# Kernel optimization log

Measured on AMD Instinct MI355X. Metric: run time of the kernel, lower is better.

## Reference

```python
import jax, jax.numpy as jnp
import numpy as np

N = 2_000_000
N_IN = 128
N_HID = 32
CT_SIZE = 16384  # n_bags(1024) * n_ct(16)
N_CT = 16


def setup_inputs() -> dict:
    key = jax.random.key(0)
    ks = jax.random.split(key, 10)
    X = jax.random.normal(ks[0], (N, N_IN), dtype=jnp.float32)
    batch = jax.random.randint(ks[1], (N,), 0, CT_SIZE, dtype=jnp.int32)
    s = 1.0 / np.sqrt(N_IN)
    W1 = jax.random.uniform(ks[2], (N_IN, N_HID), jnp.float32, -s, s)
    b1 = jax.random.uniform(ks[3], (N_HID,), jnp.float32, -s, s)
    s2 = 1.0 / np.sqrt(N_HID)
    wc = jax.random.uniform(ks[4], (N_HID, 1), jnp.float32, -s2, s2)
    bc = jax.random.uniform(ks[5], (1,), jnp.float32, -s2, s2)
    wct = jax.random.uniform(ks[6], (N_HID, 1), jnp.float32, -s2, s2)
    bct = jax.random.uniform(ks[7], (1,), jnp.float32, -s2, s2)
    Wout = jax.random.uniform(ks[8], (N_HID, 1), jnp.float32, -s2, s2)
    bout = jax.random.uniform(ks[9], (1,), jnp.float32, -s2, s2)
    return {"X": X, "W1": W1, "b1": b1, "wc": wc, "bc": bc,
            "wct": wct, "bct": bct, "Wout": Wout, "bout": bout,
            "batch": batch, "ct_size": CT_SIZE, "n_ct": N_CT}


def _segment_softmax(s, batch, num_segments):
    # numerically stable softmax within each segment
    m = jax.ops.segment_max(s, batch, num_segments=num_segments)
    e = jnp.exp(s - m[batch])
    denom = jax.ops.segment_sum(e, batch, num_segments=num_segments)
    return e / denom[batch]


def reference(X, W1, b1, wc, bc, wct, bct, Wout, bout, batch, ct_size, n_ct):
    # lin: Linear(n_in, n_hid) + ReLU (dropout=0 in eval)
    H = jax.nn.relu(X @ W1 + b1)                          # [N, n_hid]
    # attn1 with use_softmax: segment softmax over cells within each (bag, celltype) segment
    s = (H @ wc + bc)[:, 0]                               # [N]
    w_c = _segment_softmax(s, batch, ct_size)             # [N]
    # global_add_pool of attention-weighted features, reshape to [n_bags, n_ct, n_hid]
    P = jax.ops.segment_sum(H * w_c[:, None], batch, num_segments=ct_size)
    P = P.reshape(-1, n_ct, N_HID)                        # [B, n_ct, n_hid]
    # lin2 is empty (n_layers_lin2=0)
    # attn2: softmax over cell-type axis
    w_ct = jax.nn.softmax(P @ wct + bct, axis=1)          # [B, n_ct, 1]
    Xb = jnp.sum(P * w_ct, axis=1)                        # [B, n_hid]
    return Xb @ Wout + bout                               # [B, 1]
```

## Files before the change

### kernel.cpp

```cpp
#include <hip/hip_runtime.h>
#include <hip/hip_bf16.h>
#include <cmath>

#define NIN   128
#define NHID  32
#define CTS   16384
#define NCT   16
#define NBAGS (CTS / NCT)
#define CAP   256
#define NBLK  256
#define SEG_STRIDE 33

typedef __attribute__((ext_vector_type(8))) short bf16x8;
typedef __attribute__((ext_vector_type(4))) float f32x4;

__device__ inline ushort f2bf(float f) {
    uint x = __float_as_uint(f);
    uint r = (x + 0x7fffu + ((x >> 16) & 1u)) >> 16;
    return (ushort)r;
}
__device__ inline float bf2f(ushort b) { return __uint_as_float(((uint)b) << 16); }


__global__ __launch_bounds__(1024) void hist_kernel(
    const int* __restrict__ batch, uint* __restrict__ hist, int n, int chunk)
{
    __shared__ uint h[CTS];
    const int b = blockIdx.x;
    for (int i = threadIdx.x; i < CTS; i += 1024) h[i] = 0;
    __syncthreads();
    const int lo = b * chunk, hi = min(n, lo + chunk);
    for (int i = lo + threadIdx.x; i < hi; i += 1024)
        atomicAdd(&h[batch[i]], 1u);
    __syncthreads();
    uint* __restrict__ hb = hist + (size_t)b * CTS;
    for (int i = threadIdx.x; i < CTS; i += 1024) hb[i] = h[i];
}

__global__ __launch_bounds__(256) void prefix_kernel(
    uint* __restrict__ hist, int* __restrict__ cnt)
{
    const int s = blockIdx.x * 256 + threadIdx.x;
    if (s >= CTS) return;
    uint run = 0;
#pragma unroll 4
    for (int b = 0; b < NBLK; ++b) {
        const uint t = hist[(size_t)b * CTS + s];
        hist[(size_t)b * CTS + s] = run;
        run += t;
    }
    cnt[s * 16] = (int)run;
}

__global__ __launch_bounds__(1024) void place_kernel(
    const int* __restrict__ batch, const uint* __restrict__ hist,
    int* __restrict__ slots, int n, int chunk)
{
    __shared__ uint h[CTS];
    const int b = blockIdx.x;
    const uint* __restrict__ hb = hist + (size_t)b * CTS;
    for (int i = threadIdx.x; i < CTS; i += 1024) h[i] = hb[i];
    __syncthreads();
    const int lo = b * chunk, hi = min(n, lo + chunk);
    for (int i = lo + threadIdx.x; i < hi; i += 1024) {
        const int s = batch[i];
        const uint pos = atomicAdd(&h[s], 1u);
        if (pos < CAP) slots[(size_t)s * CAP + pos] = i;
    }
}

__global__ __launch_bounds__(256) void seg_kernel(
    const float* __restrict__ X,
    const float* __restrict__ W1,
    const float* __restrict__ b1,
    const float* __restrict__ wc,
    const float* __restrict__ bc,
    const int*   __restrict__ cnt,
    const int*   __restrict__ slots,
    float* __restrict__ P)
{
    __shared__ __align__(16) float w1s[NIN * NHID];

    const int tid = threadIdx.x;
    for (int i = tid; i < NIN * NHID / 4; i += 256)
        ((float4*)w1s)[i] = ((const float4*)W1)[i];
    __syncthreads();

    const int w    = tid >> 6;
    const int lane = tid & 63;
    const int g    = lane >> 4;
    const int c    = lane & 15;
    const int s    = blockIdx.x * 4 + w;
    const int m    = min(cnt[s * 16], CAP);

    bf16x8 Bf[4][2];
#pragma unroll
    for (int kc = 0; kc < 4; ++kc) {
#pragma unroll
        for (int nh = 0; nh < 2; ++nh) {
            union { bf16x8 v; ushort u[8]; } bh;
#pragma unroll
            for (int e = 0; e < 8; ++e)
                bh.u[e] = f2bf(w1s[(kc * 32 + g * 8 + e) * NHID + nh * 16 + c]);
            Bf[kc][nh] = bh.v;
        }
    }

    const float b1c0 = b1[c], b1c1 = b1[c + 16];
    const float wc0  = wc[c], wc1  = wc[c + 16];
    const float bc0  = bc[0];

    float pacc0 = 0.f, pacc1 = 0.f, esum = 0.f;
    const int ntiles = (m + 15) >> 4;
    const size_t sbase = (size_t)s * CAP;

    auto slot_of = [&](int t) -> int {
        const int ti = t * 16 + c;
        return slots[sbase + min(ti, m - 1)];
    };

    auto compute_tile = [&](const float4* x, int t) {
        f32x4 acc0 = {0.f, 0.f, 0.f, 0.f};
        f32x4 acc1 = {0.f, 0.f, 0.f, 0.f};
#pragma unroll
        for (int kc = 0; kc < 4; ++kc) {
            const float xs[8] = {x[2*kc].x, x[2*kc].y, x[2*kc].z, x[2*kc].w,
                                 x[2*kc+1].x, x[2*kc+1].y, x[2*kc+1].z, x[2*kc+1].w};
            union { bf16x8 v; __hip_bfloat162 h2[4]; } ah, al;
            float lo[8];
#pragma unroll
            for (int e = 0; e < 4; ++e) {
                const __hip_bfloat162 hb =
                    __float22bfloat162_rn(make_float2(xs[2*e], xs[2*e+1]));
                ah.h2[e] = hb;
                lo[2*e]   = xs[2*e]   - __bfloat162float(hb.x);
                lo[2*e+1] = xs[2*e+1] - __bfloat162float(hb.y);
            }
#pragma unroll
            for (int e = 0; e < 4; ++e)
                al.h2[e] = __float22bfloat162_rn(make_float2(lo[2*e], lo[2*e+1]));

            acc0 = __builtin_amdgcn_mfma_f32_16x16x32_bf16(ah.v, Bf[kc][0], acc0, 0, 0, 0);
            acc0 = __builtin_amdgcn_mfma_f32_16x16x32_bf16(al.v, Bf[kc][0], acc0, 0, 0, 0);
            acc1 = __builtin_amdgcn_mfma_f32_16x16x32_bf16(ah.v, Bf[kc][1], acc1, 0, 0, 0);
            acc1 = __builtin_amdgcn_mfma_f32_16x16x32_bf16(al.v, Bf[kc][1], acc1, 0, 0, 0);
        }
#pragma unroll
        for (int i = 0; i < 4; ++i) {
            const float h0 = fmaxf(acc0[i] + b1c0, 0.f);
            const float h1 = fmaxf(acc1[i] + b1c1, 0.f);
            float sp = h0 * wc0 + h1 * wc1;
            sp += __shfl_xor(sp, 1);
            sp += __shfl_xor(sp, 2);
            sp += __shfl_xor(sp, 4);
            sp += __shfl_xor(sp, 8);
            const int row = t * 16 + g * 4 + i;
            const float e = (row < m) ? expf(sp + bc0) : 0.f;
            pacc0 = fmaf(e, h0, pacc0);
            pacc1 = fmaf(e, h1, pacc1);
            esum += e;
        }
    };

    auto load_tile = [&](float4* x, int r) {
        const float4* __restrict__ xr = (const float4*)(X + (size_t)r * NIN);
#pragma unroll
        for (int kc = 0; kc < 4; ++kc) {
            x[2*kc]   = xr[kc * 8 + g * 2];
            x[2*kc+1] = xr[kc * 8 + g * 2 + 1];
        }
    };

    if (ntiles > 0) {
        float4 xa[8];
        load_tile(xa, slot_of(0));
        int rnext = (ntiles > 1) ? slot_of(1) : 0;

        for (int t = 0; t < ntiles; ++t) {
            float4 xb[8];
            const bool more = (t + 1) < ntiles;
            if (more) load_tile(xb, rnext);
            const int rnn = (t + 2 < ntiles) ? slot_of(t + 2) : 0;
            compute_tile(xa, t);
#pragma unroll
            for (int q = 0; q < 8; ++q) xa[q] = xb[q];
            rnext = rnn;
        }
    }

    pacc0 += __shfl_xor(pacc0, 16); pacc0 += __shfl_xor(pacc0, 32);
    pacc1 += __shfl_xor(pacc1, 16); pacc1 += __shfl_xor(pacc1, 32);
    esum  += __shfl_xor(esum, 16);  esum  += __shfl_xor(esum, 32);

    if (lane < 16) {
        const float inv = esum > 0.f ? 1.f / esum : 0.f;
        P[(size_t)s * NHID + c]      = pacc0 * inv;
        P[(size_t)s * NHID + 16 + c] = pacc1 * inv;
    }
}

__global__ __launch_bounds__(256) void bags_kernel(
    const float* __restrict__ P,
    const float* __restrict__ wct,
    const float* __restrict__ bct,
    const float* __restrict__ Wout,
    const float* __restrict__ bout,
    float* __restrict__ out)
{
    const int b = blockIdx.x * blockDim.x + threadIdx.x;
    if (b >= NBAGS) return;

    float logit[NCT], dout[NCT];
#pragma unroll
    for (int ct = 0; ct < NCT; ++ct) {
        const float* p = P + (size_t)(b * NCT + ct) * NHID;
        float t = 0.f, d = 0.f;
#pragma unroll
        for (int j = 0; j < NHID; ++j) {
            const float pj = p[j];
            t += pj * wct[j];
            d += pj * Wout[j];
        }
        logit[ct] = t + bct[0];
        dout[ct]  = d;
    }

    float mx = logit[0];
#pragma unroll
    for (int ct = 1; ct < NCT; ++ct) mx = fmaxf(mx, logit[ct]);
    float den = 0.f, accv = 0.f;
#pragma unroll
    for (int ct = 0; ct < NCT; ++ct) {
        const float e = expf(logit[ct] - mx);
        den += e;
        accv += e * dout[ct];
    }
    out[b] = accv / den + bout[0];
}


__global__ __launch_bounds__(256) void rows_kernel_atomic(
    const float* __restrict__ X, const float* __restrict__ W1,
    const float* __restrict__ b1, const float* __restrict__ wc,
    const float* __restrict__ bc, const int* __restrict__ batch,
    float* __restrict__ segacc, int n)
{
    const long long r0 = (long long)blockIdx.x * 256 + threadIdx.x;
    if (r0 >= n) return;
    const float4* xp = (const float4*)(X + (size_t)r0 * NIN);
    float acc[NHID];
#pragma unroll
    for (int j = 0; j < NHID; ++j) acc[j] = 0.f;
#pragma unroll 4
    for (int kc = 0; kc < NIN / 4; ++kc) {
        const float4 xv = xp[kc];
        const float xa[4] = {xv.x, xv.y, xv.z, xv.w};
#pragma unroll
        for (int kk = 0; kk < 4; ++kk) {
            const float* wrow = W1 + (kc * 4 + kk) * NHID;
            const float u = xa[kk];
#pragma unroll
            for (int j = 0; j < NHID; ++j) acc[j] = fmaf(u, wrow[j], acc[j]);
        }
    }
    float sc = bc[0];
#pragma unroll
    for (int j = 0; j < NHID; ++j) {
        const float h = fmaxf(acc[j] + b1[j], 0.f); acc[j] = h; sc += h * wc[j];
    }
    const float e = expf(sc);
    float* p = segacc + (size_t)batch[r0] * SEG_STRIDE;
#pragma unroll
    for (int j = 0; j < NHID; ++j) atomicAdd(p + j, e * acc[j]);
    atomicAdd(p + NHID, e);
}

__global__ __launch_bounds__(256) void bags_kernel_fb(
    const float* __restrict__ segacc, const float* __restrict__ wct,
    const float* __restrict__ bct, const float* __restrict__ Wout,
    const float* __restrict__ bout, float* __restrict__ out)
{
    const int b = blockIdx.x * blockDim.x + threadIdx.x;
    if (b >= NBAGS) return;
    float logit[NCT], dout[NCT];
#pragma unroll
    for (int ct = 0; ct < NCT; ++ct) {
        const float* p = segacc + (size_t)(b * NCT + ct) * SEG_STRIDE;
        const float den = p[NHID];
        const float inv = den > 0.f ? 1.f / den : 0.f;
        float t = 0.f, d = 0.f;
#pragma unroll
        for (int j = 0; j < NHID; ++j) { const float pj = p[j]*inv; t += pj*wct[j]; d += pj*Wout[j]; }
        logit[ct] = t + bct[0];
        dout[ct]  = d;
    }
    float mx = logit[0];
#pragma unroll
    for (int ct = 1; ct < NCT; ++ct) mx = fmaxf(mx, logit[ct]);
    float den = 0.f, accv = 0.f;
#pragma unroll
    for (int ct = 0; ct < NCT; ++ct) {
        const float e = expf(logit[ct] - mx);
        den += e; accv += e * dout[ct];
    }
    out[b] = accv / den + bout[0];
}


extern "C" void kernel_launch(void* const* d_in, const int* in_sizes, int n_in,
                              void* d_out, int out_size, void* d_ws, size_t ws_size,
                              hipStream_t stream)
{
    const float* X    = (const float*)d_in[0];
    const float* W1   = (const float*)d_in[1];
    const float* b1   = (const float*)d_in[2];
    const float* wc   = (const float*)d_in[3];
    const float* bc   = (const float*)d_in[4];
    const float* wct  = (const float*)d_in[5];
    const float* bct  = (const float*)d_in[6];
    const float* Wout = (const float*)d_in[7];
    const float* bout = (const float*)d_in[8];
    const int*   batch= (const int*)d_in[9];
    const int n = in_sizes[9];

    const size_t cnt_bytes  = (size_t)CTS * 16 * sizeof(int);
    const size_t slot_bytes = (size_t)CTS * CAP * sizeof(int);
    const size_t p_bytes    = (size_t)CTS * NHID * sizeof(float);
    const size_t hist_bytes = (size_t)NBLK * CTS * sizeof(uint);
    const size_t need = cnt_bytes + slot_bytes + p_bytes + hist_bytes;

    if (ws_size >= need) {
        int*   cnt   = (int*)d_ws;
        int*   slots = cnt + (size_t)CTS * 16;
        float* P     = (float*)(slots + (size_t)CTS * CAP);
        uint*  hist  = (uint*)(P + (size_t)CTS * NHID);

        const int chunk = (n + NBLK - 1) / NBLK;
        hist_kernel<<<NBLK, 1024, 0, stream>>>(batch, hist, n, chunk);
        prefix_kernel<<<CTS / 256, 256, 0, stream>>>(hist, cnt);
        place_kernel<<<NBLK, 1024, 0, stream>>>(batch, hist, slots, n, chunk);
        seg_kernel<<<CTS / 4, 256, 0, stream>>>(X, W1, b1, wc, bc, cnt, slots, P);
        bags_kernel<<<(NBAGS + 255) / 256, 256, 0, stream>>>(
            P, wct, bct, Wout, bout, (float*)d_out);
    } else {
        float* segacc = (float*)d_ws;
        hipMemsetAsync(segacc, 0, (size_t)CTS * SEG_STRIDE * sizeof(float), stream);
        rows_kernel_atomic<<<(n + 255) / 256, 256, 0, stream>>>(
            X, W1, b1, wc, bc, batch, segacc, n);
        bags_kernel_fb<<<(NBAGS + 255) / 256, 256, 0, stream>>>(
            segacc, wct, bct, Wout, bout, (float*)d_out);
    }
}
```

Baseline: 298.8 us.

## Stream X coalesced, scatter bf16 hidden rows by segment, reduce per segment

The segment-gather GEMM is replaced by three steps. A grid-stride kernel reads X rows in order and computes H with MFMA. It then scatters bf16 H rows into a segment-sorted buffer using global positions from an exclusive scan of the segment counts. A separate reduce kernel computes the softmax-weighted pool per segment from the compact sorted buffer. This swaps random 512B-row gathers of X for sequential reads plus small 64B scattered writes, at the cost of an extra pass over the N×32 bf16 buffer, rounding H to bf16, and an additional scan kernel. It also drops the CAP truncation on segment size.

Measured after the change: 374.9 us. +25.4%, slower.

```diff
diff --git a/kernel.cpp b/kernel.cpp
--- a/kernel.cpp
+++ b/kernel.cpp
@@ -7,7 +7,6 @@
 #define CTS   16384
 #define NCT   16
 #define NBAGS (CTS / NCT)
-#define CAP   256
 #define NBLK  256
 #define SEG_STRIDE 33
 
@@ -49,35 +48,57 @@
         hist[(size_t)b * CTS + s] = run;
         run += t;
     }
-    cnt[s * 16] = (int)run;
-}
-
-__global__ __launch_bounds__(1024) void place_kernel(
+    cnt[s] = (int)run;
+}
+
+__global__ __launch_bounds__(1024) void scan_kernel(
+    const int* __restrict__ cnt, int* __restrict__ segstart)
+{
+    __shared__ int wsum[16];
+    const int t = threadIdx.x;
+    const int base = t * 16;
+    int loc[16];
+    int run = 0;
+#pragma unroll
+    for (int i = 0; i < 16; ++i) { loc[i] = run; run += cnt[base + i]; }
+    const int lane = t & 63, wid = t >> 6;
+    int v = run;
+#pragma unroll
+    for (int d = 1; d < 64; d <<= 1) {
+        const int u = __shfl_up(v, d);
+        if (lane >= d) v += u;
+    }
+    if (lane == 63) wsum[wid] = v;
+    __syncthreads();
+    int wbase = 0;
+    for (int q = 0; q < wid; ++q) wbase += wsum[q];
+    const int excl = wbase + v - run;
+#pragma unroll
+    for (int i = 0; i < 16; ++i) segstart[base + i] = excl + loc[i];
+}
+
+__global__ __launch_bounds__(1024) void gpos_kernel(
     const int* __restrict__ batch, const uint* __restrict__ hist,
-    int* __restrict__ slots, int n, int chunk)
+    const int* __restrict__ segstart, uint* __restrict__ gpos, int n, int chunk)
 {
     __shared__ uint h[CTS];
     const int b = blockIdx.x;
     const uint* __restrict__ hb = hist + (size_t)b * CTS;
-    for (int i = threadIdx.x; i < CTS; i += 1024) h[i] = hb[i];
+    for (int i = threadIdx.x; i < CTS; i += 1024)
+        h[i] = hb[i] + (uint)segstart[i];
     __syncthreads();
     const int lo = b * chunk, hi = min(n, lo + chunk);
-    for (int i = lo + threadIdx.x; i < hi; i += 1024) {
-        const int s = batch[i];
-        const uint pos = atomicAdd(&h[s], 1u);
-        if (pos < CAP) slots[(size_t)s * CAP + pos] = i;
-    }
-}
-
-__global__ __launch_bounds__(256) void seg_kernel(
+    for (int i = lo + threadIdx.x; i < hi; i += 1024)
+        gpos[i] = atomicAdd(&h[batch[i]], 1u);
+}
+
+__global__ __launch_bounds__(256) void stream_kernel(
     const float* __restrict__ X,
     const float* __restrict__ W1,
     const float* __restrict__ b1,
-    const float* __restrict__ wc,
-    const float* __restrict__ bc,
-    const int*   __restrict__ cnt,
-    const int*   __restrict__ slots,
-    float* __restrict__ P)
+    const uint*  __restrict__ gpos,
+    ushort* __restrict__ Hb,
+    int n)
 {
     __shared__ __align__(16) float w1s[NIN * NHID];
 
@@ -90,8 +111,6 @@
     const int lane = tid & 63;
     const int g    = lane >> 4;
     const int c    = lane & 15;
-    const int s    = blockIdx.x * 4 + w;
-    const int m    = min(cnt[s * 16], CAP);
 
     bf16x8 Bf[4][2];
 #pragma unroll
@@ -107,19 +126,22 @@
     }
 
     const float b1c0 = b1[c], b1c1 = b1[c + 16];
-    const float wc0  = wc[c], wc1  = wc[c + 16];
-    const float bc0  = bc[0];
-
-    float pacc0 = 0.f, pacc1 = 0.f, esum = 0.f;
-    const int ntiles = (m + 15) >> 4;
-    const size_t sbase = (size_t)s * CAP;
-
-    auto slot_of = [&](int t) -> int {
-        const int ti = t * 16 + c;
-        return slots[sbase + min(ti, m - 1)];
+
+    const int ntiles = (n + 15) >> 4;
+    const int wid    = blockIdx.x * 4 + w;
+    const int nwaves = gridDim.x * 4;
+
+    auto load_tile = [&](float4* x, int T) {
+        const int row = min(T * 16 + c, n - 1);
+        const float4* __restrict__ xr = (const float4*)(X + (size_t)row * NIN);
+#pragma unroll
+        for (int kc = 0; kc < 4; ++kc) {
+            x[2*kc]   = xr[kc * 8 + g * 2];
+            x[2*kc+1] = xr[kc * 8 + g * 2 + 1];
+        }
     };
 
-    auto compute_tile = [&](const float4* x, int t) {
+    auto compute_tile = [&](const float4* x, int T) {
         f32x4 acc0 = {0.f, 0.f, 0.f, 0.f};
         f32x4 acc1 = {0.f, 0.f, 0.f, 0.f};
 #pragma unroll
@@ -147,55 +169,76 @@
         }
 #pragma unroll
         for (int i = 0; i < 4; ++i) {
+            const int row = T * 16 + g * 4 + i;
             const float h0 = fmaxf(acc0[i] + b1c0, 0.f);
             const float h1 = fmaxf(acc1[i] + b1c1, 0.f);
-            float sp = h0 * wc0 + h1 * wc1;
-            sp += __shfl_xor(sp, 1);
-            sp += __shfl_xor(sp, 2);
-            sp += __shfl_xor(sp, 4);
-            sp += __shfl_xor(sp, 8);
-            const int row = t * 16 + g * 4 + i;
-            const float e = (row < m) ? expf(sp + bc0) : 0.f;
-            pacc0 = fmaf(e, h0, pacc0);
-            pacc1 = fmaf(e, h1, pacc1);
-            esum += e;
+            const __hip_bfloat162 hb = __float22bfloat162_rn(make_float2(h0, h1));
+            if (row < n) {
+                const uint gp = gpos[row];
+                *(uint*)((char*)Hb + ((size_t)gp << 6) + 4 * c) =
+                    *(const uint*)&hb;
+            }
         }
     };
 
-    auto load_tile = [&](float4* x, int r) {
-        const float4* __restrict__ xr = (const float4*)(X + (size_t)r * NIN);
-#pragma unroll
-        for (int kc = 0; kc < 4; ++kc) {
-            x[2*kc]   = xr[kc * 8 + g * 2];
-            x[2*kc+1] = xr[kc * 8 + g * 2 + 1];
-        }
-    };
-
-    if (ntiles > 0) {
+    int T = wid;
+    if (T < ntiles) {
         float4 xa[8];
-        load_tile(xa, slot_of(0));
-        int rnext = (ntiles > 1) ? slot_of(1) : 0;
-
-        for (int t = 0; t < ntiles; ++t) {
+        load_tile(xa, T);
+        while (T < ntiles) {
+            const int Tn = T + nwaves;
             float4 xb[8];
-            const bool more = (t + 1) < ntiles;
-            if (more) load_tile(xb, rnext);
-            const int rnn = (t + 2 < ntiles) ? slot_of(t + 2) : 0;
-            compute_tile(xa, t);
+            if (Tn < ntiles) load_tile(xb, Tn);
+            compute_tile(xa, T);
 #pragma unroll
             for (int q = 0; q < 8; ++q) xa[q] = xb[q];
-            rnext = rnn;
-        }
-    }
-
-    pacc0 += __shfl_xor(pacc0, 16); pacc0 += __shfl_xor(pacc0, 32);
-    pacc1 += __shfl_xor(pacc1, 16); pacc1 += __shfl_xor(pacc1, 32);
-    esum  += __shfl_xor(esum, 16);  esum  += __shfl_xor(esum, 32);
+            T = Tn;
+        }
+    }
+}
+
+__global__ __launch_bounds__(256) void reduce_kernel(
+    const ushort* __restrict__ Hb,
+    const int* __restrict__ cnt,
+    const int* __restrict__ segstart,
+    const float* __restrict__ wc,
+    const float* __restrict__ bc,
+    float* __restrict__ P)
+{
+    const int tid  = threadIdx.x;
+    const int w    = tid >> 6;
+    const int lane = tid & 63;
+    const int rg   = lane >> 4;
+    const int c    = lane & 15;
+    const int s    = blockIdx.x * 4 + w;
+    const int m    = cnt[s];
+    const int base = segstart[s];
+    const float wc0 = wc[c], wc1 = wc[c + 16], bc0 = bc[0];
+
+    float a0 = 0.f, a1 = 0.f, es = 0.f;
+    for (int j = rg; j < m; j += 4) {
+        const uint pk = *(const uint*)((const char*)Hb +
+                                       ((size_t)(base + j) << 6) + 4 * c);
+        const float h0 = bf2f((ushort)(pk & 0xffffu));
+        const float h1 = bf2f((ushort)(pk >> 16));
+        float sp = h0 * wc0 + h1 * wc1;
+        sp += __shfl_xor(sp, 1);
+        sp += __shfl_xor(sp, 2);
+        sp += __shfl_xor(sp, 4);
+        sp += __shfl_xor(sp, 8);
+        const float e = expf(sp + bc0);
+        a0 = fmaf(e, h0, a0);
+        a1 = fmaf(e, h1, a1);
+        es += e;
+    }
+    a0 += __shfl_xor(a0, 16); a0 += __shfl_xor(a0, 32);
+    a1 += __shfl_xor(a1, 16); a1 += __shfl_xor(a1, 32);
+    es += __shfl_xor(es, 16); es += __shfl_xor(es, 32);
 
     if (lane < 16) {
-        const float inv = esum > 0.f ? 1.f / esum : 0.f;
-        P[(size_t)s * NHID + c]      = pacc0 * inv;
-        P[(size_t)s * NHID + 16 + c] = pacc1 * inv;
+        const float inv = es > 0.f ? 1.f / es : 0.f;
+        float2 pv = make_float2(a0 * inv, a1 * inv);
+        *(float2*)&P[(size_t)s * NHID + 2 * c] = pv;
     }
 }
 
@@ -217,9 +260,10 @@
         float t = 0.f, d = 0.f;
 #pragma unroll
         for (int j = 0; j < NHID; ++j) {
+            const int dim = (j >> 1) + ((j & 1) << 4);
             const float pj = p[j];
-            t += pj * wct[j];
-            d += pj * Wout[j];
+            t += pj * wct[dim];
+            d += pj * Wout[dim];
         }
         logit[ct] = t + bct[0];
         dout[ct]  = d;
@@ -323,23 +367,31 @@
     const int*   batch= (const int*)d_in[9];
     const int n = in_sizes[9];
 
-    const size_t cnt_bytes  = (size_t)CTS * 16 * sizeof(int);
-    const size_t slot_bytes = (size_t)CTS * CAP * sizeof(int);
+    const size_t cnt_bytes  = (size_t)CTS * sizeof(int);
+    const size_t ss_bytes   = (size_t)CTS * sizeof(int);
+    const size_t gpos_bytes = (size_t)n * sizeof(uint);
     const size_t p_bytes    = (size_t)CTS * NHID * sizeof(float);
     const size_t hist_bytes = (size_t)NBLK * CTS * sizeof(uint);
-    const size_t need = cnt_bytes + slot_bytes + p_bytes + hist_bytes;
+    const size_t hb_bytes   = (size_t)n * NHID * sizeof(ushort);
+    const size_t need = cnt_bytes + ss_bytes + gpos_bytes + p_bytes
+                      + hist_bytes + hb_bytes;
 
     if (ws_size >= need) {
-        int*   cnt   = (int*)d_ws;
-        int*   slots = cnt + (size_t)CTS * 16;
-        float* P     = (float*)(slots + (size_t)CTS * CAP);
-        uint*  hist  = (uint*)(P + (size_t)CTS * NHID);
+        char* p0 = (char*)d_ws;
+        int*    cnt      = (int*)p0;                 p0 += cnt_bytes;
+        int*    segstart = (int*)p0;                 p0 += ss_bytes;
+        uint*   gpos     = (uint*)p0;                p0 += gpos_bytes;
+        float*  P        = (float*)p0;               p0 += p_bytes;
+        uint*   hist     = (uint*)p0;                p0 += hist_bytes;
+        ushort* Hb       = (ushort*)p0;
 
         const int chunk = (n + NBLK - 1) / NBLK;
         hist_kernel<<<NBLK, 1024, 0, stream>>>(batch, hist, n, chunk);
         prefix_kernel<<<CTS / 256, 256, 0, stream>>>(hist, cnt);
-        place_kernel<<<NBLK, 1024, 0, stream>>>(batch, hist, slots, n, chunk);
-        seg_kernel<<<CTS / 4, 256, 0, stream>>>(X, W1, b1, wc, bc, cnt, slots, P);
+        scan_kernel<<<1, 1024, 0, stream>>>(cnt, segstart);
+        gpos_kernel<<<NBLK, 1024, 0, stream>>>(batch, hist, segstart, gpos, n, chunk);
+        stream_kernel<<<2048, 256, 0, stream>>>(X, W1, b1, gpos, Hb, n);
+        reduce_kernel<<<CTS / 4, 256, 0, stream>>>(Hb, cnt, segstart, wc, bc, P);
         bags_kernel<<<(NBAGS + 255) / 256, 256, 0, stream>>>(
             P, wct, bct, Wout, bout, (float*)d_out);
     } else {
```
